# Kernel optimization log

Hardware: AMD Instinct MI355X
Metric: run time of the kernel (lower is better)

The kernel has to match this reference:

```python
import jax, jax.numpy as jnp
import numpy as np

NUM_LABELS_I = 28  # 7 entity types * 4 (B/I/E/S)
NUM_LABELS = 31    # + O, EOS, BOS
INDEX_O, INDEX_EOS, INDEX_BOS = 28, 29, 30
NEG = -10000.0


def _make_trans(rng):
    # replicate ChainCRF4NestedNER.reset_parameters() structural masking
    bs = np.arange(0, NUM_LABELS_I, 4)
    is_ = bs + 1
    es = bs + 2
    ss = bs + 3
    t = (rng.standard_normal((NUM_LABELS, NUM_LABELS)) * 0.1).astype(np.float32)
    for i in bs:
        t[i, :i + 1] = NEG; t[i, i + 3:] = NEG
    for i in is_:
        t[i, :i] = NEG; t[i, i + 2:] = NEG
    for i in np.concatenate([es, ss, [INDEX_O]]):
        t[i, is_] = NEG; t[i, es] = NEG; t[i, INDEX_BOS] = NEG
    t[INDEX_EOS, :INDEX_EOS] = NEG; t[INDEX_EOS, INDEX_BOS] = NEG
    t[INDEX_BOS, is_] = NEG; t[INDEX_BOS, es] = NEG; t[INDEX_BOS, INDEX_BOS] = NEG
    return jnp.asarray(t)


def setup_inputs() -> dict:
    B, T, D = 64, 512, 768
    key = jax.random.key(0)
    k1, k2, k3 = jax.random.split(key, 3)
    inp = jax.random.normal(k1, (B, T, D), dtype=jnp.float32)
    target = jax.random.randint(k2, (B, T), 0, 29, dtype=jnp.int64)  # real labels + O only
    mask = jnp.ones((B, T), dtype=jnp.float32)
    state_w = jax.random.normal(k3, (NUM_LABELS, D), dtype=jnp.float32) * 0.02
    state_b = jnp.concatenate([jnp.zeros(INDEX_EOS, jnp.float32),
                               jnp.full(NUM_LABELS - INDEX_EOS, NEG, jnp.float32)])
    trans = _make_trans(np.random.default_rng(0))
    return {"input": inp, "target": target, "mask": mask,
            "state_w": state_w, "state_b": state_b, "trans": trans}


def reference(input, target, mask, state_w, state_b, trans):
    B, T, _ = input.shape
    # state scores [B, T, L]
    out_s = jnp.einsum('btd,ld->btl', input, state_w) + state_b
    out_s = out_s.at[:, :, INDEX_EOS].add((mask == 0).astype(out_s.dtype) * 20000.0)
    # energy [B, T, L, L]: trans[prev, curr] + state[curr]
    energy = trans[None, None, :, :] + out_s[:, :, None, :]
    # forward algorithm (logsumexp semiring) as a scan over time
    energy_t = jnp.moveaxis(energy, 1, 0)  # [T, B, L, L]
    part0 = energy_t[0, :, INDEX_BOS, :]   # [B, L]

    def step(part, e_t):
        new = jax.nn.logsumexp(e_t + part[:, :, None], axis=1)
        return new, None

    partition, _ = jax.lax.scan(step, part0, energy_t[1:])
    # gold-path energy: sum_t energy[b, t, prev_label, label]
    prev = jnp.concatenate([jnp.full((B, 1), INDEX_BOS, dtype=target.dtype),
                            target[:, :-1]], axis=1)
    bi = jnp.arange(B)[:, None]
    ti = jnp.arange(T)[None, :]
    tgt_energy = energy[bi, ti, prev, target].sum(axis=1)
    loss = jax.nn.logsumexp(trans[:, INDEX_EOS][None, :] + partition, axis=1) - tgt_energy
    return loss, energy
```

## Files before the change

kernel.cpp:

```cpp
#include <hip/hip_runtime.h>

typedef float f32x4  __attribute__((ext_vector_type(4)));
typedef float f32x16 __attribute__((ext_vector_type(16)));
typedef short s16x8  __attribute__((ext_vector_type(8)));

constexpr int NL  = 31;
constexpr int BB  = 64;
constexpr int TT  = 512;
constexpr int DD  = 768;
constexpr int RTOT = BB * TT;
constexpr int IDX_EOS = 29;
constexpr int IDX_BOS = 30;
constexpr float LOG2E = 1.4426950408889634f;
constexpr float LN2F  = 0.6931471805599453f;

union Frag8 { unsigned u[4]; s16x8 s; };

__device__ inline unsigned pk2(float a, float b) {
  unsigned ua = __float_as_uint(a), ub = __float_as_uint(b);
  ua = (ua + 0x7fffu + ((ua >> 16) & 1u)) >> 16;
  ub = (ub + 0x7fffu + ((ub >> 16) & 1u)) >> 16;
  return ua | (ub << 16);
}
__device__ inline unsigned short bf16r(float a) {
  unsigned ua = __float_as_uint(a);
  return (unsigned short)((ua + 0x7fffu + ((ua >> 16) & 1u)) >> 16);
}

__device__ inline float bfly_max32(float v) {
#define STEPM(K) { float o = __int_as_float(__builtin_amdgcn_ds_swizzle(__float_as_int(v), ((K) << 10) | 0x1f)); v = fmaxf(v, o); }
  STEPM(1) STEPM(2) STEPM(4) STEPM(8) STEPM(16)
#undef STEPM
  return v;
}
__device__ inline float bfly_sum32(float v) {
#define STEPS(K) { float o = __int_as_float(__builtin_amdgcn_ds_swizzle(__float_as_int(v), ((K) << 10) | 0x1f)); v = v + o; }
  STEPS(1) STEPS(2) STEPS(4) STEPS(8) STEPS(16)
#undef STEPS
  return v;
}

__device__ inline void repack(const float E[16], int h, Frag8& B1, Frag8& B2) {
  unsigned o1a = pk2(E[4 * h], E[4 * h + 1]), o1b = pk2(E[4 * h + 2], E[4 * h + 3]);
  unsigned o2a = pk2(E[8 + 4 * h], E[8 + 4 * h + 1]), o2b = pk2(E[8 + 4 * h + 2], E[8 + 4 * h + 3]);
  int hb = 4 * (1 - h);
  unsigned s1a = pk2(E[hb], E[hb + 1]),         s1b = pk2(E[hb + 2], E[hb + 3]);
  unsigned s2a = pk2(E[8 + hb], E[8 + hb + 1]), s2b = pk2(E[8 + hb + 2], E[8 + hb + 3]);
  unsigned r1a = __shfl_xor((int)s1a, 32), r1b = __shfl_xor((int)s1b, 32);
  unsigned r2a = __shfl_xor((int)s2a, 32), r2b = __shfl_xor((int)s2b, 32);
  if (h == 0) {
    B1.u[0] = o1a; B1.u[1] = o1b; B1.u[2] = r1a; B1.u[3] = r1b;
    B2.u[0] = o2a; B2.u[1] = o2b; B2.u[2] = r2a; B2.u[3] = r2b;
  } else {
    B1.u[0] = r1a; B1.u[1] = r1b; B1.u[2] = o1a; B1.u[3] = o1b;
    B2.u[0] = r2a; B2.u[1] = r2b; B2.u[2] = o2a; B2.u[3] = o2b;
  }
}

__device__ inline void renorm16(float E[16], float& Sacc) {
  float m = E[0];
#pragma unroll
  for (int r = 1; r < 16; ++r) m = fmaxf(m, E[r]);
  m = bfly_max32(m);
  m = fmaxf(m, __shfl_xor(m, 32));
  float lg = truncf(log2f(m));
  Sacc += lg;
  float sc = exp2f(-lg);
#pragma unroll
  for (int r = 0; r < 16; ++r) E[r] *= sc;
}

__device__ inline void load_A16(const unsigned short* M, int l, int h, Frag8& A1, Frag8& A2) {
  A1.s = *(const s16x8*)(M + l * 32 + 8 * h);
  A2.s = *(const s16x8*)(M + l * 32 + 16 + 8 * h);
}
__device__ inline void load_B16(const unsigned short* M, int l, int h, Frag8& B1, Frag8& B2) {
#pragma unroll
  for (int m = 0; m < 4; ++m) {
    int k = 8 * h + 2 * m;
    unsigned lo0 = M[k * 32 + l],        hi0 = M[(k + 1) * 32 + l];
    unsigned lo1 = M[(k + 16) * 32 + l], hi1 = M[(k + 17) * 32 + l];
    B1.u[m] = lo0 | (hi0 << 16);
    B2.u[m] = lo1 | (hi1 << 16);
  }
}

__device__ inline void tree_node(unsigned short* Tb, float* Ts, int ja, int jb, int l, int h) {
  Frag8 A1, A2, B1, B2;
  load_A16(Tb + ja * 1024, l, h, A1, A2);
  load_B16(Tb + jb * 1024, l, h, B1, B2);
  f32x16 D = {};
  D = __builtin_amdgcn_mfma_f32_32x32x16_bf16(A1.s, B1.s, D, 0, 0, 0);
  D = __builtin_amdgcn_mfma_f32_32x32x16_bf16(A2.s, B2.s, D, 0, 0, 0);
  float E[16];
#pragma unroll
  for (int r = 0; r < 16; ++r) E[r] = D[r];
  float S = Ts[ja] + Ts[jb];
  renorm16(E, S);
#pragma unroll
  for (int r = 0; r < 16; ++r) {
    int row = (r & 3) + 8 * (r >> 2) + 4 * h;
    Tb[jb * 1024 + row * 32 + l] = bf16r(E[r]);
  }
  if (l == 0 && h == 0) Ts[jb] = S;
}

__global__ void k_prep(const float* __restrict__ sw, unsigned short* __restrict__ Bw) {
  for (int i = blockIdx.x * 256 + threadIdx.x; i < 32 * DD; i += 8 * 256)
    Bw[i] = (i < NL * DD) ? bf16r(sw[i]) : (unsigned short)0;
}

__global__ __launch_bounds__(256) void k_fused(
    const float* __restrict__ inp, const unsigned short* __restrict__ Bw,
    const float* __restrict__ sb, const float* __restrict__ msk,
    const float* __restrict__ trans, const int* __restrict__ target,
    float* __restrict__ energy, float* __restrict__ ws_partial,
    unsigned short* __restrict__ Mb, float* __restrict__ Sb,
    float* __restrict__ out0)
{
  __shared__ float tr[961];
  __shared__ float osh[16 * NL];
  __shared__ float ubw[4][128];
  __shared__ __align__(16) unsigned short Ms[4][1024];
  __shared__ float Ss[4];
  int tid = threadIdx.x, wave = tid >> 6, lane = tid & 63;
  int bid = blockIdx.x;
  int r0 = bid * 16;

  if (wave) {
    for (int idx = tid - 64; idx < 961; idx += 192) tr[idx] = trans[idx];
  } else {
    int quad = lane >> 4, l15 = lane & 15;
    const float* arow = inp + (size_t)(r0 + l15) * DD + quad * 8;

    f32x4 pa0a = *(const f32x4*)(arow);
    f32x4 pa0b = *(const f32x4*)(arow + 4);
    f32x4 pa1a = *(const f32x4*)(arow + 32);
    f32x4 pa1b = *(const f32x4*)(arow + 36);

    f32x4 acc[2] = {};
    for (int kc = 0; kc < 12; ++kc) {
      Frag8 af0, af1;
      af0.u[0] = pk2(pa0a[0], pa0a[1]); af0.u[1] = pk2(pa0a[2], pa0a[3]);
      af0.u[2] = pk2(pa0b[0], pa0b[1]); af0.u[3] = pk2(pa0b[2], pa0b[3]);
      af1.u[0] = pk2(pa1a[0], pa1a[1]); af1.u[1] = pk2(pa1a[2], pa1a[3]);
      af1.u[2] = pk2(pa1b[0], pa1b[1]); af1.u[3] = pk2(pa1b[2], pa1b[3]);
      if (kc < 11) {
        const float* a2 = arow + (kc + 1) * 64;
        pa0a = *(const f32x4*)(a2);      pa0b = *(const f32x4*)(a2 + 4);
        pa1a = *(const f32x4*)(a2 + 32); pa1b = *(const f32x4*)(a2 + 36);
      }
#pragma unroll
      for (int ct = 0; ct < 2; ++ct) {
        s16x8 bf0 = *(const s16x8*)(Bw + (ct * 16 + l15) * DD + kc * 64 + quad * 8);
        acc[ct] = __builtin_amdgcn_mfma_f32_16x16x32_bf16(af0.s, bf0, acc[ct], 0, 0, 0);
        s16x8 bf1 = *(const s16x8*)(Bw + (ct * 16 + l15) * DD + kc * 64 + 32 + quad * 8);
        acc[ct] = __builtin_amdgcn_mfma_f32_16x16x32_bf16(af1.s, bf1, acc[ct], 0, 0, 0);
      }
    }
#pragma unroll
    for (int ct = 0; ct < 2; ++ct) {
      int n = ct * 16 + l15;
      if (n < NL) {
        float b = sb[n];
#pragma unroll
        for (int r = 0; r < 4; ++r) {
          int lr = quad * 4 + r;
          float v = acc[ct][r] + b;
          if (n == IDX_EOS && msk[r0 + lr] == 0.f) v += 20000.f;
          osh[lr * NL + n] = v;
        }
      }
    }
  }
  __syncthreads();

  if ((bid & 31) == 0 && tid < NL) out0[(bid >> 5) * NL + tid] = osh[tid];

  if (tid < 16) {
    int r = r0 + tid;
    int tg = target[r];
    int prv = ((r & (TT - 1)) == 0) ? IDX_BOS : target[r - 1];
    float cc = tr[prv * NL + tg] + osh[tid * NL + tg];
#pragma unroll
    for (int off = 8; off; off >>= 1) cc += __shfl_down(cc, off);
    if (tid == 0) ws_partial[bid] = cc;
  }

  float* dst = energy + (size_t)r0 * 961;
#pragma unroll 5
  for (int it = 0; it < 15; ++it) {
    int v = it * 256 + tid;
    int e = v * 4;
    f32x4 val;
#pragma unroll
    for (int k = 0; k < 4; ++k) {
      unsigned x = e + k;
      unsigned q = __umulhi(x, 4469269u);
      unsigned c = x - q * 961u;
      unsigned j = c - 31u * ((c * 67651u) >> 21);
      val[k] = tr[c] + osh[q * NL + j];
    }
    *(f32x4*)(dst + e) = val;
  }
  if (tid < 4) {
    int e = (3840 + tid) * 4;
    f32x4 val;
#pragma unroll
    for (int k = 0; k < 4; ++k) {
      unsigned x = e + k;
      unsigned q = __umulhi(x, 4469269u);
      unsigned c = x - q * 961u;
      unsigned j = c - 31u * ((c * 67651u) >> 21);
      val[k] = tr[c] + osh[q * NL + j];
    }
    *(f32x4*)(dst + e) = val;
  }

  {
    int l = lane & 31, h = lane >> 5;
    int s0 = (bid % 32 == 0 && wave == 0) ? 1 : 0;

    float* ub = ubw[wave];
#pragma unroll
    for (int it = 0; it < 2; ++it) {
      int idx = lane + it * 64;
      int row = idx >> 5, col = idx & 31;
      float v = 0.f;
      if (col < NL) v = exp2f(LOG2E * osh[(4 * wave + row) * NL + col]);
      ub[idx] = v;
    }

    Frag8 A1, A2, B1, B2;
#pragma unroll
    for (int m = 0; m < 4; ++m) {
      int k0 = 8 * h + 2 * m, k1 = k0 + 1;
      float a0 = (k0 < NL && l < NL) ? exp2f(LOG2E * tr[k0 * NL + l]) : 0.f;
      float a1 = (k1 < NL && l < NL) ? exp2f(LOG2E * tr[k1 * NL + l]) : 0.f;
      A1.u[m] = pk2(a0, a1);
      int k2 = 16 + k0, k3 = 16 + k1;
      float a2 = (k2 < NL && l < NL) ? exp2f(LOG2E * tr[k2 * NL + l]) : 0.f;
      float a3 = (k3 < NL && l < NL) ? exp2f(LOG2E * tr[k3 * NL + l]) : 0.f;
      A2.u[m] = pk2(a2, a3);
      B1.u[m] = ((k0 == l) ? 0x3f80u : 0u) | (((k1 == l) ? 0x3f80u : 0u) << 16);
      B2.u[m] = ((k2 == l) ? 0x3f80u : 0u) | (((k3 == l) ? 0x3f80u : 0u) << 16);
    }

    float E[16];
    for (int s = s0; s < 4; ++s) {
      const float* us = ub + s * 32 + 4 * h;
      f32x4 u0 = *(const f32x4*)(us);
      f32x4 u1 = *(const f32x4*)(us + 8);
      f32x4 u2 = *(const f32x4*)(us + 16);
      f32x4 u3 = *(const f32x4*)(us + 24);
      f32x16 D = {};
      D = __builtin_amdgcn_mfma_f32_32x32x16_bf16(A1.s, B1.s, D, 0, 0, 0);
      D = __builtin_amdgcn_mfma_f32_32x32x16_bf16(A2.s, B2.s, D, 0, 0, 0);
#pragma unroll
      for (int jj = 0; jj < 4; ++jj) {
        E[jj]      = D[jj]      * u0[jj];
        E[4 + jj]  = D[4 + jj]  * u1[jj];
        E[8 + jj]  = D[8 + jj]  * u2[jj];
        E[12 + jj] = D[12 + jj] * u3[jj];
      }
      if (s < 3) repack(E, h, B1, B2);
    }
    float S = 0.f;
    renorm16(E, S);
    unsigned short* mo = Ms[wave];
#pragma unroll
    for (int r = 0; r < 16; ++r) {
      int row = (r & 3) + 8 * (r >> 2) + 4 * h;
      mo[row * 32 + l] = bf16r(E[r]);
    }
    if (lane == 0) Ss[wave] = S;
  }
  __syncthreads();

  if (wave == 0) {
    int l = lane & 31, h = lane >> 5;
    Frag8 A1, A2, B1, B2;
    load_B16(Ms[0], l, h, B1, B2);
    float Sx = Ss[0] + Ss[1] + Ss[2] + Ss[3];
    float E2[16];
#pragma unroll
    for (int i = 1; i < 4; ++i) {
      load_A16(Ms[i], l, h, A1, A2);
      f32x16 D = {};
      D = __builtin_amdgcn_mfma_f32_32x32x16_bf16(A1.s, B1.s, D, 0, 0, 0);
      D = __builtin_amdgcn_mfma_f32_32x32x16_bf16(A2.s, B2.s, D, 0, 0, 0);
#pragma unroll
      for (int r = 0; r < 16; ++r) E2[r] = D[r];
      if (i < 3) repack(E2, h, B1, B2);
    }
    renorm16(E2, Sx);
    unsigned short* qo = Mb + (size_t)bid * 1024;
#pragma unroll
    for (int r = 0; r < 16; ++r) {
      int row = (r & 3) + 8 * (r >> 2) + 4 * h;
      qo[row * 32 + l] = bf16r(E2[r]);
    }
    if (lane == 0) Sb[bid] = Sx;
  }
}

__global__ __launch_bounds__(256) void k_tree(
    const float* __restrict__ trans, const unsigned short* __restrict__ Mb,
    const float* __restrict__ Sb, const float* __restrict__ ws_partial,
    const float* __restrict__ out0, float* __restrict__ loss)
{
  __shared__ __align__(16) unsigned short T[32][1024];
  __shared__ float Ts[32];
  __shared__ float wsh[32];
  int tid = threadIdx.x, wave = tid >> 6, lane = tid & 63;
  int l = lane & 31, h = lane >> 5;
  int b = blockIdx.x;

  const f32x4* src = (const f32x4*)(Mb + (size_t)b * 32 * 1024);
  f32x4* dstT = (f32x4*)T;
#pragma unroll
  for (int i = 0; i < 16; ++i) dstT[tid + i * 256] = src[tid + i * 256];
  if (tid < 32) {
    Ts[tid] = Sb[b * 32 + tid];
    wsh[tid] = ws_partial[b * 32 + tid];
  }
  __syncthreads();

  unsigned short* T0 = T[0];
#pragma unroll
  for (int i = 0; i < 4; ++i) { int j = wave + 4 * i; tree_node(T0, Ts, 2 * j + 1, 2 * j, l, h); }
  __syncthreads();
#pragma unroll
  for (int i = 0; i < 2; ++i) { int j = wave + 4 * i; tree_node(T0, Ts, 4 * j + 2, 4 * j, l, h); }
  __syncthreads();
  { int j = wave; tree_node(T0, Ts, 8 * j + 4, 8 * j, l, h); }
  __syncthreads();
  if (wave < 2) { int j = wave; tree_node(T0, Ts, 16 * j + 8, 16 * j, l, h); }
  __syncthreads();

  if (wave == 0) {
    Frag8 A1, A2, B1, B2;
    load_A16(T0 + 16 * 1024, l, h, A1, A2);
    load_B16(T0, l, h, B1, B2);
    f32x16 D = {};
    D = __builtin_amdgcn_mfma_f32_32x32x16_bf16(A1.s, B1.s, D, 0, 0, 0);
    D = __builtin_amdgcn_mfma_f32_32x32x16_bf16(A2.s, B2.s, D, 0, 0, 0);
    float E[16];
#pragma unroll
    for (int r = 0; r < 16; ++r) E[r] = D[r];
    float S = Ts[0] + Ts[16];

    float p0 = (l < NL) ? exp2f(LOG2E * (trans[IDX_BOS * NL + l] + out0[b * NL + l])) : 0.f;
    float sum_h = 0.f;
#pragma unroll
    for (int r = 0; r < 16; ++r) {
      float s = bfly_sum32(E[r] * p0);
      int row = (r & 3) + 8 * (r >> 2) + 4 * h;
      float We = (row < NL) ? exp2f(LOG2E * trans[row * NL + IDX_EOS]) : 0.f;
      sum_h += s * We;
    }
    float tot = sum_h + __shfl_xor(sum_h, 32);
    if (lane == 0) {
      float wst = 0.f;
#pragma unroll
      for (int i = 0; i < 32; ++i) wst += wsh[i];
      loss[b] = LN2F * (S + log2f(tot)) - wst;
    }
  }
}

extern "C" void kernel_launch(void* const* d_in, const int* in_sizes, int n_in,
                              void* d_out, int out_size, void* d_ws, size_t ws_size,
                              hipStream_t stream) {
  const float* inp   = (const float*)d_in[0];
  const int*   tgt   = (const int*)d_in[1];
  const float* msk   = (const float*)d_in[2];
  const float* sw    = (const float*)d_in[3];
  const float* sb    = (const float*)d_in[4];
  const float* trans = (const float*)d_in[5];

  float* out    = (float*)d_out;
  float* loss   = out;
  float* energy = out + BB;

  float* ws_partial = (float*)d_ws;
  float* Sb   = ws_partial + 2048;
  float* out0 = Sb + 2048;
  unsigned short* Mb = (unsigned short*)(out0 + 2048);
  unsigned short* Bw = Mb + (size_t)2048 * 1024;

  k_prep<<<8, 256, 0, stream>>>(sw, Bw);
  k_fused<<<RTOT / 16, 256, 0, stream>>>(inp, Bw, sb, msk, trans, tgt,
                                         energy, ws_partial, Mb, Sb, out0);
  k_tree<<<BB, 256, 0, stream>>>(trans, Mb, Sb, ws_partial, out0, loss);
}
```

Baseline: 264.2 us.

## Specialize waves: one wave runs serial 16-step MFMA chain, others write energy

The per-block 16-step transfer-matrix product now runs in wave 0 as a single serial chain, renormalising every four steps. The old four-wave split with an LDS tree combine and its extra barrier is gone. Waves 1-3 write the energy tensor concurrently using incremental index arithmetic instead of per-element divisions, and the gold-path partial moves to wave 1. Launch bounds request 8 blocks per CU and LDS use shrinks. The cost is a longer serial MFMA dependency chain in one wave, and the energy stores are now spread over 192 threads instead of 256.

```diff
diff --git a/kernel.cpp b/kernel.cpp
--- a/kernel.cpp
+++ b/kernel.cpp
@@ -110,7 +110,7 @@
     Bw[i] = (i < NL * DD) ? bf16r(sw[i]) : (unsigned short)0;
 }
 
-__global__ __launch_bounds__(256) void k_fused(
+__global__ __launch_bounds__(256, 8) void k_fused(
     const float* __restrict__ inp, const unsigned short* __restrict__ Bw,
     const float* __restrict__ sb, const float* __restrict__ msk,
     const float* __restrict__ trans, const int* __restrict__ target,
@@ -120,9 +120,6 @@
 {
   __shared__ float tr[961];
   __shared__ float osh[16 * NL];
-  __shared__ float ubw[4][128];
-  __shared__ __align__(16) unsigned short Ms[4][1024];
-  __shared__ float Ss[4];
   int tid = threadIdx.x, wave = tid >> 6, lane = tid & 63;
   int bid = blockIdx.x;
   int r0 = bid * 16;
@@ -177,59 +174,9 @@
 
   if ((bid & 31) == 0 && tid < NL) out0[(bid >> 5) * NL + tid] = osh[tid];
 
-  if (tid < 16) {
-    int r = r0 + tid;
-    int tg = target[r];
-    int prv = ((r & (TT - 1)) == 0) ? IDX_BOS : target[r - 1];
-    float cc = tr[prv * NL + tg] + osh[tid * NL + tg];
-#pragma unroll
-    for (int off = 8; off; off >>= 1) cc += __shfl_down(cc, off);
-    if (tid == 0) ws_partial[bid] = cc;
-  }
-
-  float* dst = energy + (size_t)r0 * 961;
-#pragma unroll 5
-  for (int it = 0; it < 15; ++it) {
-    int v = it * 256 + tid;
-    int e = v * 4;
-    f32x4 val;
-#pragma unroll
-    for (int k = 0; k < 4; ++k) {
-      unsigned x = e + k;
-      unsigned q = __umulhi(x, 4469269u);
-      unsigned c = x - q * 961u;
-      unsigned j = c - 31u * ((c * 67651u) >> 21);
-      val[k] = tr[c] + osh[q * NL + j];
-    }
-    *(f32x4*)(dst + e) = val;
-  }
-  if (tid < 4) {
-    int e = (3840 + tid) * 4;
-    f32x4 val;
-#pragma unroll
-    for (int k = 0; k < 4; ++k) {
-      unsigned x = e + k;
-      unsigned q = __umulhi(x, 4469269u);
-      unsigned c = x - q * 961u;
-      unsigned j = c - 31u * ((c * 67651u) >> 21);
-      val[k] = tr[c] + osh[q * NL + j];
-    }
-    *(f32x4*)(dst + e) = val;
-  }
-
-  {
+  if (wave == 0) {
     int l = lane & 31, h = lane >> 5;
-    int s0 = (bid % 32 == 0 && wave == 0) ? 1 : 0;
-
-    float* ub = ubw[wave];
-#pragma unroll
-    for (int it = 0; it < 2; ++it) {
-      int idx = lane + it * 64;
-      int row = idx >> 5, col = idx & 31;
-      float v = 0.f;
-      if (col < NL) v = exp2f(LOG2E * osh[(4 * wave + row) * NL + col]);
-      ub[idx] = v;
-    }
+    int s0 = ((bid & 31) == 0) ? 1 : 0;
 
     Frag8 A1, A2, B1, B2;
 #pragma unroll
@@ -247,60 +194,74 @@
     }
 
     float E[16];
-    for (int s = s0; s < 4; ++s) {
-      const float* us = ub + s * 32 + 4 * h;
-      f32x4 u0 = *(const f32x4*)(us);
-      f32x4 u1 = *(const f32x4*)(us + 8);
-      f32x4 u2 = *(const f32x4*)(us + 16);
-      f32x4 u3 = *(const f32x4*)(us + 24);
+    float S = 0.f;
+    for (int s = s0; s < 16; ++s) {
       f32x16 D = {};
       D = __builtin_amdgcn_mfma_f32_32x32x16_bf16(A1.s, B1.s, D, 0, 0, 0);
       D = __builtin_amdgcn_mfma_f32_32x32x16_bf16(A2.s, B2.s, D, 0, 0, 0);
 #pragma unroll
-      for (int jj = 0; jj < 4; ++jj) {
-        E[jj]      = D[jj]      * u0[jj];
-        E[4 + jj]  = D[4 + jj]  * u1[jj];
-        E[8 + jj]  = D[8 + jj]  * u2[jj];
-        E[12 + jj] = D[12 + jj] * u3[jj];
-      }
-      if (s < 3) repack(E, h, B1, B2);
-    }
-    float S = 0.f;
-    renorm16(E, S);
-    unsigned short* mo = Ms[wave];
+      for (int t = 0; t < 4; ++t) {
+#pragma unroll
+        for (int jj = 0; jj < 4; ++jj) {
+          int col = t * 8 + 4 * h + jj;
+          float u = (col < NL) ? exp2f(LOG2E * osh[s * NL + col]) : 0.f;
+          E[4 * t + jj] = D[4 * t + jj] * u;
+        }
+      }
+      if ((s & 3) == 3) renorm16(E, S);
+      if (s < 15) repack(E, h, B1, B2);
+    }
+    unsigned short* mo = Mb + (size_t)bid * 1024;
 #pragma unroll
     for (int r = 0; r < 16; ++r) {
       int row = (r & 3) + 8 * (r >> 2) + 4 * h;
       mo[row * 32 + l] = bf16r(E[r]);
     }
-    if (lane == 0) Ss[wave] = S;
-  }
-  __syncthreads();
-
-  if (wave == 0) {
-    int l = lane & 31, h = lane >> 5;
-    Frag8 A1, A2, B1, B2;
-    load_B16(Ms[0], l, h, B1, B2);
-    float Sx = Ss[0] + Ss[1] + Ss[2] + Ss[3];
-    float E2[16];
-#pragma unroll
-    for (int i = 1; i < 4; ++i) {
-      load_A16(Ms[i], l, h, A1, A2);
-      f32x16 D = {};
-      D = __builtin_amdgcn_mfma_f32_32x32x16_bf16(A1.s, B1.s, D, 0, 0, 0);
-      D = __builtin_amdgcn_mfma_f32_32x32x16_bf16(A2.s, B2.s, D, 0, 0, 0);
-#pragma unroll
-      for (int r = 0; r < 16; ++r) E2[r] = D[r];
-      if (i < 3) repack(E2, h, B1, B2);
-    }
-    renorm16(E2, Sx);
-    unsigned short* qo = Mb + (size_t)bid * 1024;
-#pragma unroll
-    for (int r = 0; r < 16; ++r) {
-      int row = (r & 3) + 8 * (r >> 2) + 4 * h;
-      qo[row * 32 + l] = bf16r(E2[r]);
-    }
-    if (lane == 0) Sb[bid] = Sx;
+    if (lane == 0) Sb[bid] = S;
+  } else {
+    if (wave == 1 && lane < 16) {
+      int r = r0 + lane;
+      int tg = target[r];
+      int prv = ((r & (TT - 1)) == 0) ? IDX_BOS : target[r - 1];
+      float cc = tr[prv * NL + tg] + osh[lane * NL + tg];
+#pragma unroll
+      for (int off = 8; off; off >>= 1) cc += __shfl_down(cc, off);
+      if (lane == 0) ws_partial[bid] = cc;
+    }
+
+    float* dst = energy + (size_t)r0 * 961;
+    int v0 = tid - 64;
+    unsigned c = (unsigned)(v0 * 4);
+    unsigned j = c - 31u * ((c * 67651u) >> 21);
+    unsigned oq = j;
+    for (int it = 0; it < 20; ++it) {
+      unsigned cc = c, jj = j, qq = oq;
+      f32x4 val;
+#pragma unroll
+      for (int k = 0; k < 4; ++k) {
+        val[k] = tr[cc] + osh[qq];
+        ++cc; ++jj; ++qq;
+        if (jj == 31u) { jj = 0u; qq -= 31u; }
+        if (cc == 961u) { cc = 0u; qq += 31u; }
+      }
+      *(f32x4*)(dst + it * 768 + v0 * 4) = val;
+      c += 768u; j += 24u; oq += 24u;
+      if (j >= 31u) { j -= 31u; oq -= 31u; }
+      if (c >= 961u) { c -= 961u; oq += 31u; }
+    }
+    if (v0 < 4) {
+      int e = (3840 + v0) * 4;
+      f32x4 val;
+#pragma unroll
+      for (int k = 0; k < 4; ++k) {
+        unsigned x = e + k;
+        unsigned q = __umulhi(x, 4469269u);
+        unsigned cx = x - q * 961u;
+        unsigned jx = cx - 31u * ((cx * 67651u) >> 21);
+        val[k] = tr[cx] + osh[q * NL + jx];
+      }
+      *(f32x4*)(dst + e) = val;
+    }
   }
 }
 
```

After: 286.5 us. +8.4%, slower.

## Split GEMM K across all waves and overlap energy writes with tree reduction

Applied to the files above, without the earlier changes.

The state-score GEMM was done by wave 0 alone while the other waves only loaded trans. Now each of the four waves handles a quarter of K, and the partial sums are reduced through a shared buffer that is unioned with Ms. The energy output write moves after the scan product, with waves 1-3 writing 15 rows while wave 0 does the final matrix chain and then writes 1 row. The energy write also uses a duplicated osh row layout so each row can be produced with contiguous vector loads of trans, avoiding per-element div/mod. Adds an extra barrier and reduction, raises the occupancy hint to 8, and leaves energy stores unbalanced across waves.

```diff
diff --git a/kernel.cpp b/kernel.cpp
--- a/kernel.cpp
+++ b/kernel.cpp
@@ -105,12 +105,34 @@
   if (l == 0 && h == 0) Ts[jb] = S;
 }
 
+__device__ inline void energy_rows(float* dst0, const float* tr_p, const float* osh,
+                                   int rbeg, int rend, int lane) {
+  for (int r = rbeg; r < rend; ++r) {
+    float* drow = dst0 + (size_t)r * 961;
+    const float* orow = osh + r * 64;
+#pragma unroll
+    for (int it = 0; it < 4; ++it) {
+      int e = it * 256 + lane * 4;
+      if (e <= 957) {
+        f32x4 t4 = *(const f32x4*)(tr_p + e);
+        unsigned j = (unsigned)e - 31u * (((unsigned)e * 67651u) >> 21);
+        f32x4 val;
+#pragma unroll
+        for (int k = 0; k < 4; ++k) val[k] = t4[k] + orow[j + k];
+        *(f32x4*)(drow + e) = val;
+      } else if (e == 960) {
+        drow[960] = tr_p[960] + orow[30];
+      }
+    }
+  }
+}
+
 __global__ void k_prep(const float* __restrict__ sw, unsigned short* __restrict__ Bw) {
   for (int i = blockIdx.x * 256 + threadIdx.x; i < 32 * DD; i += 8 * 256)
     Bw[i] = (i < NL * DD) ? bf16r(sw[i]) : (unsigned short)0;
 }
 
-__global__ __launch_bounds__(256) void k_fused(
+__global__ __launch_bounds__(256, 8) void k_fused(
     const float* __restrict__ inp, const unsigned short* __restrict__ Bw,
     const float* __restrict__ sb, const float* __restrict__ msk,
     const float* __restrict__ trans, const int* __restrict__ target,
@@ -118,116 +140,89 @@
     unsigned short* __restrict__ Mb, float* __restrict__ Sb,
     float* __restrict__ out0)
 {
-  __shared__ float tr[961];
-  __shared__ float osh[16 * NL];
-  __shared__ float ubw[4][128];
-  __shared__ __align__(16) unsigned short Ms[4][1024];
+  __shared__ __align__(16) union {
+    float accbuf[4][16][33];
+    unsigned short Ms[4][1024];
+  } ovl;
+  __shared__ __align__(16) float tr_p[964];
+  __shared__ __align__(16) float osh[16 * 64];
+  __shared__ __align__(16) float ubw[4][128];
   __shared__ float Ss[4];
+
   int tid = threadIdx.x, wave = tid >> 6, lane = tid & 63;
   int bid = blockIdx.x;
   int r0 = bid * 16;
-
-  if (wave) {
-    for (int idx = tid - 64; idx < 961; idx += 192) tr[idx] = trans[idx];
-  } else {
-    int quad = lane >> 4, l15 = lane & 15;
-    const float* arow = inp + (size_t)(r0 + l15) * DD + quad * 8;
-
+  int quad = lane >> 4, l15 = lane & 15;
+
+  {
+    int kcb = 3 * wave;
+    const float* arow = inp + (size_t)(r0 + l15) * DD + kcb * 64 + quad * 8;
     f32x4 pa0a = *(const f32x4*)(arow);
     f32x4 pa0b = *(const f32x4*)(arow + 4);
     f32x4 pa1a = *(const f32x4*)(arow + 32);
     f32x4 pa1b = *(const f32x4*)(arow + 36);
 
     f32x4 acc[2] = {};
-    for (int kc = 0; kc < 12; ++kc) {
+#pragma unroll
+    for (int kc = 0; kc < 3; ++kc) {
       Frag8 af0, af1;
       af0.u[0] = pk2(pa0a[0], pa0a[1]); af0.u[1] = pk2(pa0a[2], pa0a[3]);
       af0.u[2] = pk2(pa0b[0], pa0b[1]); af0.u[3] = pk2(pa0b[2], pa0b[3]);
       af1.u[0] = pk2(pa1a[0], pa1a[1]); af1.u[1] = pk2(pa1a[2], pa1a[3]);
       af1.u[2] = pk2(pa1b[0], pa1b[1]); af1.u[3] = pk2(pa1b[2], pa1b[3]);
-      if (kc < 11) {
+      if (kc < 2) {
         const float* a2 = arow + (kc + 1) * 64;
         pa0a = *(const f32x4*)(a2);      pa0b = *(const f32x4*)(a2 + 4);
         pa1a = *(const f32x4*)(a2 + 32); pa1b = *(const f32x4*)(a2 + 36);
       }
 #pragma unroll
       for (int ct = 0; ct < 2; ++ct) {
-        s16x8 bf0 = *(const s16x8*)(Bw + (ct * 16 + l15) * DD + kc * 64 + quad * 8);
+        const unsigned short* bp = Bw + (ct * 16 + l15) * DD + (kcb + kc) * 64 + quad * 8;
+        s16x8 bf0 = *(const s16x8*)(bp);
         acc[ct] = __builtin_amdgcn_mfma_f32_16x16x32_bf16(af0.s, bf0, acc[ct], 0, 0, 0);
-        s16x8 bf1 = *(const s16x8*)(Bw + (ct * 16 + l15) * DD + kc * 64 + 32 + quad * 8);
+        s16x8 bf1 = *(const s16x8*)(bp + 32);
         acc[ct] = __builtin_amdgcn_mfma_f32_16x16x32_bf16(af1.s, bf1, acc[ct], 0, 0, 0);
       }
     }
 #pragma unroll
-    for (int ct = 0; ct < 2; ++ct) {
-      int n = ct * 16 + l15;
-      if (n < NL) {
-        float b = sb[n];
-#pragma unroll
-        for (int r = 0; r < 4; ++r) {
-          int lr = quad * 4 + r;
-          float v = acc[ct][r] + b;
-          if (n == IDX_EOS && msk[r0 + lr] == 0.f) v += 20000.f;
-          osh[lr * NL + n] = v;
-        }
+    for (int ct = 0; ct < 2; ++ct)
+#pragma unroll
+      for (int r = 0; r < 4; ++r)
+        ovl.accbuf[wave][quad * 4 + r][ct * 16 + l15] = acc[ct][r];
+  }
+  __syncthreads();
+
+  {
+#pragma unroll
+    for (int u = 0; u < 2; ++u) {
+      int v = tid * 2 + u;
+      int lr = v >> 5, col = v & 31;
+      if (col < NL) {
+        float s = ovl.accbuf[0][lr][col] + ovl.accbuf[1][lr][col]
+                + ovl.accbuf[2][lr][col] + ovl.accbuf[3][lr][col];
+        s += sb[col];
+        if (col == IDX_EOS && msk[r0 + lr] == 0.f) s += 20000.f;
+        osh[lr * 64 + col] = s;
+        osh[lr * 64 + 31 + col] = s;
       }
     }
+    for (int idx = tid; idx < 964; idx += 256) tr_p[idx] = (idx < 961) ? trans[idx] : 0.f;
   }
   __syncthreads();
 
   if ((bid & 31) == 0 && tid < NL) out0[(bid >> 5) * NL + tid] = osh[tid];
 
-  if (tid < 16) {
-    int r = r0 + tid;
-    int tg = target[r];
-    int prv = ((r & (TT - 1)) == 0) ? IDX_BOS : target[r - 1];
-    float cc = tr[prv * NL + tg] + osh[tid * NL + tg];
-#pragma unroll
-    for (int off = 8; off; off >>= 1) cc += __shfl_down(cc, off);
-    if (tid == 0) ws_partial[bid] = cc;
-  }
-
-  float* dst = energy + (size_t)r0 * 961;
-#pragma unroll 5
-  for (int it = 0; it < 15; ++it) {
-    int v = it * 256 + tid;
-    int e = v * 4;
-    f32x4 val;
-#pragma unroll
-    for (int k = 0; k < 4; ++k) {
-      unsigned x = e + k;
-      unsigned q = __umulhi(x, 4469269u);
-      unsigned c = x - q * 961u;
-      unsigned j = c - 31u * ((c * 67651u) >> 21);
-      val[k] = tr[c] + osh[q * NL + j];
-    }
-    *(f32x4*)(dst + e) = val;
-  }
-  if (tid < 4) {
-    int e = (3840 + tid) * 4;
-    f32x4 val;
-#pragma unroll
-    for (int k = 0; k < 4; ++k) {
-      unsigned x = e + k;
-      unsigned q = __umulhi(x, 4469269u);
-      unsigned c = x - q * 961u;
-      unsigned j = c - 31u * ((c * 67651u) >> 21);
-      val[k] = tr[c] + osh[q * NL + j];
-    }
-    *(f32x4*)(dst + e) = val;
-  }
+  int l = lane & 31, h = lane >> 5;
 
   {
-    int l = lane & 31, h = lane >> 5;
-    int s0 = (bid % 32 == 0 && wave == 0) ? 1 : 0;
-
+    int s0 = ((bid & 31) == 0 && wave == 0) ? 1 : 0;
     float* ub = ubw[wave];
 #pragma unroll
     for (int it = 0; it < 2; ++it) {
       int idx = lane + it * 64;
       int row = idx >> 5, col = idx & 31;
       float v = 0.f;
-      if (col < NL) v = exp2f(LOG2E * osh[(4 * wave + row) * NL + col]);
+      if (col < NL) v = exp2f(LOG2E * osh[(4 * wave + row) * 64 + col]);
       ub[idx] = v;
     }
 
@@ -235,12 +230,12 @@
 #pragma unroll
     for (int m = 0; m < 4; ++m) {
       int k0 = 8 * h + 2 * m, k1 = k0 + 1;
-      float a0 = (k0 < NL && l < NL) ? exp2f(LOG2E * tr[k0 * NL + l]) : 0.f;
-      float a1 = (k1 < NL && l < NL) ? exp2f(LOG2E * tr[k1 * NL + l]) : 0.f;
+      float a0 = (k0 < NL && l < NL) ? exp2f(LOG2E * tr_p[k0 * NL + l]) : 0.f;
+      float a1 = (k1 < NL && l < NL) ? exp2f(LOG2E * tr_p[k1 * NL + l]) : 0.f;
       A1.u[m] = pk2(a0, a1);
       int k2 = 16 + k0, k3 = 16 + k1;
-      float a2 = (k2 < NL && l < NL) ? exp2f(LOG2E * tr[k2 * NL + l]) : 0.f;
-      float a3 = (k3 < NL && l < NL) ? exp2f(LOG2E * tr[k3 * NL + l]) : 0.f;
+      float a2 = (k2 < NL && l < NL) ? exp2f(LOG2E * tr_p[k2 * NL + l]) : 0.f;
+      float a3 = (k3 < NL && l < NL) ? exp2f(LOG2E * tr_p[k3 * NL + l]) : 0.f;
       A2.u[m] = pk2(a2, a3);
       B1.u[m] = ((k0 == l) ? 0x3f80u : 0u) | (((k1 == l) ? 0x3f80u : 0u) << 16);
       B2.u[m] = ((k2 == l) ? 0x3f80u : 0u) | (((k3 == l) ? 0x3f80u : 0u) << 16);
@@ -267,7 +262,7 @@
     }
     float S = 0.f;
     renorm16(E, S);
-    unsigned short* mo = Ms[wave];
+    unsigned short* mo = ovl.Ms[wave];
 #pragma unroll
     for (int r = 0; r < 16; ++r) {
       int row = (r & 3) + 8 * (r >> 2) + 4 * h;
@@ -278,14 +273,13 @@
   __syncthreads();
 
   if (wave == 0) {
-    int l = lane & 31, h = lane >> 5;
     Frag8 A1, A2, B1, B2;
-    load_B16(Ms[0], l, h, B1, B2);
+    load_B16(ovl.Ms[0], l, h, B1, B2);
     float Sx = Ss[0] + Ss[1] + Ss[2] + Ss[3];
     float E2[16];
 #pragma unroll
     for (int i = 1; i < 4; ++i) {
-      load_A16(Ms[i], l, h, A1, A2);
+      load_A16(ovl.Ms[i], l, h, A1, A2);
       f32x16 D = {};
       D = __builtin_amdgcn_mfma_f32_32x32x16_bf16(A1.s, B1.s, D, 0, 0, 0);
       D = __builtin_amdgcn_mfma_f32_32x32x16_bf16(A2.s, B2.s, D, 0, 0, 0);
@@ -301,6 +295,20 @@
       qo[row * 32 + l] = bf16r(E2[r]);
     }
     if (lane == 0) Sb[bid] = Sx;
+
+    energy_rows(energy + (size_t)r0 * 961, tr_p, osh, 15, 16, lane);
+  } else {
+    if (wave == 1 && lane < 16) {
+      int r = r0 + lane;
+      int tg = target[r];
+      int prv = ((r & (TT - 1)) == 0) ? IDX_BOS : target[r - 1];
+      float cc = tr_p[prv * NL + tg] + osh[lane * 64 + tg];
+#pragma unroll
+      for (int off = 8; off; off >>= 1) cc += __shfl_down(cc, off);
+      if (lane == 0) ws_partial[bid] = cc;
+    }
+    int rb = 5 * (wave - 1);
+    energy_rows(energy + (size_t)r0 * 961, tr_p, osh, rb, rb + 5, lane);
   }
 }
 
```

New measurement: 294.5 us. +11.5%, slower.
